# Kernel tuning notes

Hardware: AMD Instinct MI355X
Metric: run time of the kernel (lower is better)

Reference implementation:

```python
import jax, jax.numpy as jnp
import numpy as np

R = 2          # pool ratio -> context window = R * P
P = 8          # patch_size
STRIDE = 8     # window_stride
NH = 8         # n_heads
EPS = 1e-6


def _partition_nonoverlap(x, ws):
    # (N,C,H,W) -> (N*nH*nW, C, ws, ws), matches F.unfold path with padding 0
    n, c, h, w = x.shape
    x = x.reshape(n, c, h // ws, ws, w // ws, ws)
    x = jnp.transpose(x, (0, 2, 4, 1, 3, 5))
    return x.reshape(-1, c, ws, ws)


def _partition_overlap(x, ws, stride):
    # (N,C,H,W) -> (N*nH*nW, C, ws, ws) with padding (ws-stride)//2, matching F.unfold
    n, c, h, w = x.shape
    pad = (ws - stride) // 2
    xp = jnp.pad(x, ((0, 0), (0, 0), (pad, pad), (pad, pad)))
    ih = (jnp.arange(h // stride) * stride)[:, None] + jnp.arange(ws)[None, :]
    iw = (jnp.arange(w // stride) * stride)[:, None] + jnp.arange(ws)[None, :]
    xw = xp[:, :, ih, :]          # (n, c, nH, ws, Wp)
    xw = xw[:, :, :, :, iw]       # (n, c, nH, ws, nW, ws)
    xw = jnp.transpose(xw, (0, 2, 4, 1, 3, 5))  # (n, nH, nW, c, ws, ws)
    return xw.reshape(-1, c, ws, ws)


def setup_inputs() -> dict:
    key = jax.random.key(0)
    ks = jax.random.split(key, 4)
    C = 512
    x = jax.random.normal(ks[0], (1, C, 128, 128), jnp.float32)
    ln_w = jnp.ones((C,), jnp.float32)
    ln_b = jnp.zeros((C,), jnp.float32)
    mix_w = jax.random.normal(ks[1], (NH, P * P, P * P), jnp.float32) * 0.02
    mix_b = jnp.zeros((NH, P * P), jnp.float32)
    in_w = jax.random.normal(ks[2], (3 * C, C), jnp.float32) * 0.02
    in_b = jnp.zeros((3 * C,), jnp.float32)
    out_w = jax.random.normal(ks[3], (C, C), jnp.float32) * 0.02
    out_b = jnp.zeros((C,), jnp.float32)
    return dict(x=x, ln_w=ln_w, ln_b=ln_b, mix_w=mix_w, mix_b=mix_b,
                in_w=in_w, in_b=in_b, out_w=out_w, out_b=out_b)


def reference(x, ln_w, ln_b, mix_w, mix_b, in_w, in_b, out_w, out_b):
    n, c, h, w = x.shape
    ws = R * P
    L = P * P  # 64 positions per window

    # query windows: non-overlapping 8x8 patches -> (B, L, C)
    q = _partition_nonoverlap(x, P)
    q = q.reshape(-1, c, L).transpose(0, 2, 1)

    # context windows: 16x16 overlapping, avg-pooled r x r -> 8x8 -> (B, L, C)
    ctx = _partition_overlap(x, ws, STRIDE)
    ctx = ctx.reshape(-1, c, P, R, P, R).mean(axis=(3, 5))  # AvgPool2d(r, r)
    ctx = ctx.reshape(-1, c, L).transpose(0, 2, 1)

    # LayerNorm over channel dim (eps 1e-6, biased variance)
    mu = ctx.mean(-1, keepdims=True)
    var = ctx.var(-1, keepdims=True)
    ctx = (ctx - mu) / jnp.sqrt(var + EPS) * ln_w + ln_b

    # PositionMixing: per-head Linear(64,64) over the L axis + residual
    B = ctx.shape[0]
    t = ctx.transpose(0, 2, 1).reshape(B, NH, c // NH, L)  # (B, H, hd, L)
    mixed = jnp.einsum('bhcl,hml->bhcm', t, mix_w) + mix_b[None, :, None, :]
    ctx = (t + mixed).reshape(B, c, L).transpose(0, 2, 1)  # (B, L, C)

    # nn.MultiheadAttention with batch_first=False (torch default):
    # first dim B (windows) is the SEQUENCE, second dim L=64 is the BATCH.
    hd = c // NH
    Wq, Wk, Wv = in_w[:c], in_w[c:2 * c], in_w[2 * c:]
    bq, bk, bv = in_b[:c], in_b[c:2 * c], in_b[2 * c:]
    Q = (jnp.einsum('slc,ec->sle', q, Wq) + bq).reshape(B, L, NH, hd)
    K = (jnp.einsum('slc,ec->sle', ctx, Wk) + bk).reshape(B, L, NH, hd)
    V = (jnp.einsum('slc,ec->sle', ctx, Wv) + bv).reshape(B, L, NH, hd)
    scale = 1.0 / jnp.sqrt(jnp.asarray(hd, x.dtype))
    scores = jnp.einsum('slhd,tlhd->lhst', Q, K) * scale  # (L, H, B, B)
    attn = jax.nn.softmax(scores, axis=-1)
    o = jnp.einsum('lhst,tlhd->slhd', attn, V).reshape(B, L, c)
    o = jnp.einsum('slc,ec->sle', o, out_w) + out_b

    # nlc_to_nchw + window_reverse -> (N, C, H, W)
    o = o.transpose(0, 2, 1).reshape(B, c, P, P)
    o = o.reshape(n, h // P, w // P, c, P, P)
    o = jnp.transpose(o, (0, 3, 1, 4, 2, 5)).reshape(n, c, h, w)
    return o
```

## Files before the change

kernel.cpp:

```cpp
#include <hip/hip_runtime.h>


typedef __bf16 bf16;
typedef __bf16 bf16x2 __attribute__((ext_vector_type(2)));
typedef __bf16 bf16x4 __attribute__((ext_vector_type(4)));
typedef __bf16 bf16x8 __attribute__((ext_vector_type(8)));
typedef float f32x4 __attribute__((ext_vector_type(4)));

#define MFMA(a, b, c) __builtin_amdgcn_mfma_f32_16x16x32_bf16(a, b, c, 0, 0, 0)

__device__ __forceinline__ void gll16(const void* g, void* l) {
  __builtin_amdgcn_global_load_lds((const __attribute__((address_space(1))) void*)g,
                                   (__attribute__((address_space(3))) void*)l, 16, 0, 0);
}

__global__ void k_wconv(const float* __restrict__ in_w, const float* __restrict__ out_w,
                        bf16* __restrict__ wib, bf16* __restrict__ wob) {
  int i = blockIdx.x * blockDim.x + threadIdx.x;
  const int n1 = (1536 * 512) / 4;
  float4 v;
  bf16* dst;
  if (i < n1) { v = ((const float4*)in_w)[i];      dst = wib + (size_t)i * 4; }
  else        { v = ((const float4*)out_w)[i - n1]; dst = wob + (size_t)(i - n1) * 4; }
  dst[0] = (bf16)v.x; dst[1] = (bf16)v.y; dst[2] = (bf16)v.z; dst[3] = (bf16)v.w;
}

__global__ __launch_bounds__(256) void k_pq(const float* __restrict__ x,
                                            float* __restrict__ xp2t,
                                            bf16* __restrict__ qb) {
  __shared__ float xs[2][64][133];
  const int y2 = blockIdx.x, c0 = blockIdx.y * 64, t = threadIdx.x;
  #pragma unroll
  for (int it = 0; it < 16; ++it) {
    int flat = it * 256 + t;
    int ci = flat >> 6, rest = flat & 63;
    int yb = rest >> 5, xq = rest & 31;
    float4 v = *(const float4*)(x + (size_t)(c0 + ci) * 16384 +
                                (size_t)(2 * y2 + yb) * 128 + xq * 4);
    float* d = &xs[yb][ci][xq * 4];
    d[0] = v.x; d[1] = v.y; d[2] = v.z; d[3] = v.w;
  }
  __syncthreads();
  #pragma unroll
  for (int it = 0; it < 16; ++it) {
    int flat = it * 256 + t;
    int x2 = flat >> 6, ci = flat & 63;
    float s = xs[0][ci][2 * x2] + xs[0][ci][2 * x2 + 1] +
              xs[1][ci][2 * x2] + xs[1][ci][2 * x2 + 1];
    xp2t[(size_t)(y2 * 64 + x2) * 512 + c0 + ci] = 0.25f * s;
  }
  #pragma unroll
  for (int yb = 0; yb < 2; ++yb) {
    const int Y = 2 * y2 + yb;
    const int hy = Y >> 3, py = Y & 7;
    #pragma unroll
    for (int it = 0; it < 32; ++it) {
      int flat = it * 256 + t;
      int X = flat >> 6, ci = flat & 63;
      int l = py * 8 + (X & 7), s = hy * 16 + (X >> 3);
      qb[((size_t)l * 256 + s) * 512 + c0 + ci] = (bf16)xs[yb][ci][X];
    }
  }
}

__global__ __launch_bounds__(512) void k_ln(const float* __restrict__ xp2t,
                                            const float* __restrict__ lnw,
                                            const float* __restrict__ lnb,
                                            bf16* __restrict__ T) {
  __shared__ bf16 Tt[512][24];
  const int s = blockIdx.x, qt = blockIdx.y;
  const int wy = s >> 4, wx = s & 15;
  const int t = threadIdx.x, wv = t >> 6, ln = t & 63;

  float wl[8], bl[8];
  #pragma unroll
  for (int k = 0; k < 8; ++k) { wl[k] = lnw[k * 64 + ln]; bl[k] = lnb[k * 64 + ln]; }

  float v[2][8], mu_[2], rs_[2];
  #pragma unroll
  for (int p = 0; p < 2; ++p) {
    const int l = qt * 16 + wv * 2 + p;
    const int py = l >> 3, px = l & 7;
    const int y2 = wy * 4 - 2 + py, x2 = wx * 4 - 2 + px;
    const bool inb = (y2 >= 0) && (y2 < 64) && (x2 >= 0) && (x2 < 64);
    const float* src = xp2t + (size_t)(y2 * 64 + x2) * 512;
    float sum = 0.f, ssq = 0.f;
    #pragma unroll
    for (int k = 0; k < 8; ++k) {
      float xv = 0.f;
      if (inb) xv = src[k * 64 + ln];
      v[p][k] = xv; sum += xv; ssq += xv * xv;
    }
    #pragma unroll
    for (int off = 1; off < 64; off <<= 1) {
      sum += __shfl_xor(sum, off);
      ssq += __shfl_xor(ssq, off);
    }
    float mu = sum * (1.f / 512.f);
    mu_[p] = mu;
    rs_[p] = rsqrtf(ssq * (1.f / 512.f) - mu * mu + 1e-6f);
  }
  #pragma unroll
  for (int k = 0; k < 8; ++k) {
    const int c = k * 64 + ln;
    bf16x2 u;
    u.x = (bf16)((v[0][k] - mu_[0]) * rs_[0] * wl[k] + bl[k]);
    u.y = (bf16)((v[1][k] - mu_[1]) * rs_[1] * wl[k] + bl[k]);
    *(bf16x2*)(&Tt[c][wv * 2]) = u;
  }
  __syncthreads();
  #pragma unroll
  for (int it = 0; it < 2; ++it) {
    int flat = it * 512 + t;
    int c = flat >> 1, ch = flat & 1;
    bf16x8 u = *(const bf16x8*)(&Tt[c][ch * 8]);
    *(bf16x8*)(T + ((size_t)s * 512 + c) * 64 + qt * 16 + ch * 8) = u;
  }
}

__global__ __launch_bounds__(256) void k_mix(const bf16* __restrict__ T,
                                             const float* __restrict__ mix_w,
                                             const float* __restrict__ mix_b,
                                             bf16* __restrict__ ctx) {
  const int t = threadIdx.x, wv = t >> 6, ln = t & 63;
  const int s = blockIdx.x, hg = blockIdx.y;
  const int h = hg * 4 + wv;
  const int q = ln >> 4, r = ln & 15;

  bf16x8 a[4][2];
  #pragma unroll
  for (int m = 0; m < 4; ++m) {
    #pragma unroll
    for (int ks = 0; ks < 2; ++ks) {
      const int rm = m * 16 + r;
      const float* wsrc = mix_w + ((size_t)h * 64 + rm) * 64 + ks * 32 + q * 8;
      bf16x8 pk;
      #pragma unroll
      for (int e = 0; e < 8; ++e) {
        int l = ks * 32 + q * 8 + e;
        float w = wsrc[e] + (rm == l ? 1.f : 0.f);
        pk[e] = (bf16)w;
      }
      a[m][ks] = pk;
    }
  }
  const bf16* Tb = T + ((size_t)s * 512 + h * 64) * 64;
  bf16x8 b[4][2];
  #pragma unroll
  for (int n = 0; n < 4; ++n) {
    #pragma unroll
    for (int ks = 0; ks < 2; ++ks)
      b[n][ks] = *(const bf16x8*)(Tb + (size_t)(n * 16 + r) * 64 + ks * 32 + q * 8);
  }
  f32x4 acc[4][4] = {};
  #pragma unroll
  for (int ks = 0; ks < 2; ++ks) {
    #pragma unroll
    for (int m = 0; m < 4; ++m) {
      #pragma unroll
      for (int n = 0; n < 4; ++n) acc[m][n] = MFMA(a[m][ks], b[n][ks], acc[m][n]);
    }
  }
  #pragma unroll
  for (int m = 0; m < 4; ++m) {
    #pragma unroll
    for (int j = 0; j < 4; ++j) {
      const int rm = m * 16 + q * 4 + j;
      const float bias = mix_b[h * 64 + rm];
      #pragma unroll
      for (int n = 0; n < 4; ++n)
        ctx[((size_t)rm * 256 + s) * 512 + h * 64 + n * 16 + r] =
            (bf16)(acc[m][n][j] + bias);
    }
  }
}

template <int MODE>
__global__ __launch_bounds__(256, 3) void k_gemm(const bf16* __restrict__ A,
                                                 const bf16* __restrict__ B,
                                                 const float* __restrict__ bias,
                                                 bf16* __restrict__ O0,
                                                 bf16* __restrict__ O1) {
  __shared__ bf16 As[4096];
  __shared__ bf16 Bs[4096];
  const int t = threadIdx.x, wv = t >> 6, ln = t & 63;
  const int bm = blockIdx.y, bn = blockIdx.x;
  const int wm = wv >> 1, wn = wv & 1;
  f32x4 acc[4][4] = {};

  const int srow = wv * 32 + (ln >> 2);
  const int scolb = (ln & 3) * 16;
  const char* ga = (const char*)A + ((size_t)(bm * 128 + srow) * 512) * 2 + scolb;
  const char* gb = (const char*)B + ((size_t)(bn * 128 + srow) * 512) * 2 + scolb;
  bf16* lA = As + wv * 1024;
  bf16* lB = Bs + wv * 1024;

  for (int k0 = 0; k0 < 512; k0 += 32) {
    gll16(ga + k0 * 2,             lA);
    gll16(ga + k0 * 2 + 16 * 1024, lA + 512);
    gll16(gb + k0 * 2,             lB);
    gll16(gb + k0 * 2 + 16 * 1024, lB + 512);
    __syncthreads();
    bf16x8 af[4], bfr[4];
    #pragma unroll
    for (int m = 0; m < 4; ++m)
      af[m] = *(const bf16x8*)(As + (wm * 64 + m * 16 + (ln & 15)) * 32 + (ln >> 4) * 8);
    #pragma unroll
    for (int n = 0; n < 4; ++n)
      bfr[n] = *(const bf16x8*)(Bs + (wn * 64 + n * 16 + (ln & 15)) * 32 + (ln >> 4) * 8);
    #pragma unroll
    for (int m = 0; m < 4; ++m) {
      #pragma unroll
      for (int n = 0; n < 4; ++n) acc[m][n] = MFMA(af[m], bfr[n], acc[m][n]);
    }
    __syncthreads();
  }

  const int r0 = bm * 128 + wm * 64 + (ln >> 4) * 4;
  const int c0 = bn * 128 + wn * 64 + (ln & 15);
  #pragma unroll
  for (int m = 0; m < 4; ++m) {
    const int rg0 = r0 + m * 16;
    #pragma unroll
    for (int n = 0; n < 4; ++n) {
      const int cg = c0 + n * 16;
      const float bv = bias[cg];
      if constexpr (MODE == 2) {
        #pragma unroll
        for (int j = 0; j < 4; ++j)
          O0[(size_t)(rg0 + j) * 512 + cg] = (bf16)(acc[m][n][j] + bv);
      } else if constexpr (MODE == 0) {
        const int li = rg0 >> 8;
        #pragma unroll
        for (int j = 0; j < 4; ++j) {
          int sp = (rg0 + j) & 255;
          O0[(((size_t)li * 8 + (cg >> 6)) * 256 + sp) * 64 + (cg & 63)] =
              (bf16)(acc[m][n][j] + bv);
        }
      } else {
        const int li = rg0 >> 8;
        if (cg < 512) {
          #pragma unroll
          for (int j = 0; j < 4; ++j) {
            int sp = (rg0 + j) & 255;
            O0[(((size_t)li * 8 + (cg >> 6)) * 256 + sp) * 64 + (cg & 63)] =
                (bf16)(acc[m][n][j] + bv);
          }
        } else {
          const int e = cg - 512, hh = e >> 6, d = e & 63;
          const int sp = rg0 & 255;
          bf16x4 pk;
          #pragma unroll
          for (int j = 0; j < 4; ++j) pk[j] = (bf16)(acc[m][n][j] + bv);
          *(bf16x4*)(&O1[(((size_t)li * 8 + hh) * 64 + d) * 256 + sp]) = pk;
        }
      }
    }
  }
}

__global__ __launch_bounds__(256, 4) void k_attn(const bf16* __restrict__ Qa,
                                                 const bf16* __restrict__ Ka,
                                                 const bf16* __restrict__ Vt,
                                                 bf16* __restrict__ Oa) {
  __shared__ bf16 Ks[128][68];
  __shared__ bf16 Ps[64][132];
  __shared__ float sfl[64];
  __shared__ float rrs[64];

  const int t = threadIdx.x, wv = t >> 6, ln = t & 63;
  const int q = ln >> 4, r = ln & 15;
  const int bid = blockIdx.x;
  const int st = (bid >> 3) & 3;
  const int lh = (bid & 7) | ((bid >> 5) << 3);
  const int s0 = st * 64;
  const size_t base = (size_t)lh * (256 * 64);
  const bf16* Qlh = Qa + base;
  const bf16* Klh = Ka + base;
  const bf16* Vlh = Vt + base;

  const float SC = 0.125f * 1.4426950408889634f;

  bf16x8 aq[2];
  #pragma unroll
  for (int ks = 0; ks < 2; ++ks)
    aq[ks] = *(const bf16x8*)(Qlh + (size_t)(s0 + wv * 16 + r) * 64 + ks * 32 + q * 8);

  const int krow = t >> 1, khf = (t & 1) * 32;
  {
    bf16x8 kst0[4];
    #pragma unroll
    for (int i = 0; i < 4; ++i)
      kst0[i] = *(const bf16x8*)(Klh + (size_t)krow * 64 + khf + i * 8);
    #pragma unroll
    for (int i = 0; i < 4; ++i) *(bf16x8*)(&Ks[krow][khf + i * 8]) = kst0[i];
  }
  __syncthreads();

  f32x4 ao[4] = {};
  float m4[4], l4[4];
  f32x4 acc[8];

  #pragma unroll
  for (int n = 0; n < 8; ++n) acc[n] = (f32x4){0.f, 0.f, 0.f, 0.f};
  #pragma unroll
  for (int n = 0; n < 8; ++n) {
    bf16x8 b0 = *(const bf16x8*)(&Ks[n * 16 + r][q * 8]);
    bf16x8 b1 = *(const bf16x8*)(&Ks[n * 16 + r][32 + q * 8]);
    acc[n] = MFMA(aq[0], b0, acc[n]);
    acc[n] = MFMA(aq[1], b1, acc[n]);
  }

  bf16x8 bv[4];
  #pragma unroll
  for (int ks = 0; ks < 4; ++ks)
    bv[ks] = *(const bf16x8*)(Vlh + (size_t)(wv * 16 + r) * 256 + ks * 32 + q * 8);
  bf16x8 kst[4];
  #pragma unroll
  for (int i = 0; i < 4; ++i)
    kst[i] = *(const bf16x8*)(Klh + (size_t)(128 + krow) * 64 + khf + i * 8);

  #pragma unroll
  for (int j = 0; j < 4; ++j) {
    float mx = acc[0][j];
    #pragma unroll
    for (int n = 1; n < 8; ++n) mx = fmaxf(mx, acc[n][j]);
    #pragma unroll
    for (int off = 1; off < 16; off <<= 1) mx = fmaxf(mx, __shfl_xor(mx, off));
    m4[j] = mx;
    const float ms = mx * SC;
    float sm = 0.f;
    #pragma unroll
    for (int n = 0; n < 8; ++n) {
      float p = exp2f(acc[n][j] * SC - ms);
      acc[n][j] = p;
      sm += p;
    }
    #pragma unroll
    for (int off = 1; off < 16; off <<= 1) sm += __shfl_xor(sm, off);
    l4[j] = sm;
    const int row = wv * 16 + q * 4 + j;
    #pragma unroll
    for (int n = 0; n < 8; ++n) Ps[row][n * 16 + r] = (bf16)acc[n][j];
  }
  __syncthreads();

  #pragma unroll
  for (int i = 0; i < 4; ++i) *(bf16x8*)(&Ks[krow][khf + i * 8]) = kst[i];
  #pragma unroll
  for (int ks = 0; ks < 4; ++ks) {
    #pragma unroll
    for (int m = 0; m < 4; ++m) {
      bf16x8 ap = *(const bf16x8*)(&Ps[m * 16 + r][ks * 32 + q * 8]);
      ao[m] = MFMA(ap, bv[ks], ao[m]);
    }
  }
  __syncthreads();

  #pragma unroll
  for (int n = 0; n < 8; ++n) acc[n] = (f32x4){0.f, 0.f, 0.f, 0.f};
  #pragma unroll
  for (int n = 0; n < 8; ++n) {
    bf16x8 b0 = *(const bf16x8*)(&Ks[n * 16 + r][q * 8]);
    bf16x8 b1 = *(const bf16x8*)(&Ks[n * 16 + r][32 + q * 8]);
    acc[n] = MFMA(aq[0], b0, acc[n]);
    acc[n] = MFMA(aq[1], b1, acc[n]);
  }
  #pragma unroll
  for (int ks = 0; ks < 4; ++ks)
    bv[ks] = *(const bf16x8*)(Vlh + (size_t)(wv * 16 + r) * 256 + 128 + ks * 32 + q * 8);

  float sf4[4], rr4[4];
  #pragma unroll
  for (int j = 0; j < 4; ++j) {
    float mx = acc[0][j];
    #pragma unroll
    for (int n = 1; n < 8; ++n) mx = fmaxf(mx, acc[n][j]);
    #pragma unroll
    for (int off = 1; off < 16; off <<= 1) mx = fmaxf(mx, __shfl_xor(mx, off));
    const float mn = fmaxf(m4[j], mx);
    const float sf = exp2f((m4[j] - mn) * SC);
    const float ms = mn * SC;
    float sm = 0.f;
    #pragma unroll
    for (int n = 0; n < 8; ++n) {
      float p = exp2f(acc[n][j] * SC - ms);
      acc[n][j] = p;
      sm += p;
    }
    #pragma unroll
    for (int off = 1; off < 16; off <<= 1) sm += __shfl_xor(sm, off);
    sf4[j] = sf;
    rr4[j] = 1.f / (l4[j] * sf + sm);
    const int row = wv * 16 + q * 4 + j;
    #pragma unroll
    for (int n = 0; n < 8; ++n) Ps[row][n * 16 + r] = (bf16)acc[n][j];
  }
  if (r == 0) {
    *(f32x4*)(&sfl[wv * 16 + q * 4]) = (f32x4){sf4[0], sf4[1], sf4[2], sf4[3]};
    *(f32x4*)(&rrs[wv * 16 + q * 4]) = (f32x4){rr4[0], rr4[1], rr4[2], rr4[3]};
  }
  __syncthreads();

  #pragma unroll
  for (int m = 0; m < 4; ++m) {
    f32x4 sv = *(const f32x4*)(&sfl[m * 16 + q * 4]);
    #pragma unroll
    for (int j = 0; j < 4; ++j) ao[m][j] *= sv[j];
  }
  #pragma unroll
  for (int ks = 0; ks < 4; ++ks) {
    #pragma unroll
    for (int m = 0; m < 4; ++m) {
      bf16x8 ap = *(const bf16x8*)(&Ps[m * 16 + r][ks * 32 + q * 8]);
      ao[m] = MFMA(ap, bv[ks], ao[m]);
    }
  }

  float(*FS)[68] = (float(*)[68])(&Ks[0][0]);
  #pragma unroll
  for (int m = 0; m < 4; ++m) {
    f32x4 rv = *(const f32x4*)(&rrs[m * 16 + q * 4]);
    #pragma unroll
    for (int j = 0; j < 4; ++j)
      FS[m * 16 + q * 4 + j][wv * 16 + r] = ao[m][j] * rv[j];
  }
  __syncthreads();

  {
    const int row = t >> 2, qq = t & 3;
    const float* srcp = &FS[row][qq * 16];
    bf16x8 o0, o1;
    #pragma unroll
    for (int i = 0; i < 8; ++i) o0[i] = (bf16)srcp[i];
    #pragma unroll
    for (int i = 0; i < 8; ++i) o1[i] = (bf16)srcp[8 + i];
    bf16* dst = Oa + ((size_t)(lh >> 3) * 256 + s0 + row) * 512 + (lh & 7) * 64 + qq * 16;
    *(bf16x8*)(dst) = o0;
    *(bf16x8*)(dst + 8) = o1;
  }
}

__global__ void k_orelay(const bf16* __restrict__ o_tmp, float* __restrict__ out) {
  __shared__ bf16 buf[64][130];
  const int hy = blockIdx.x, py = blockIdx.y, e0 = blockIdx.z * 64, t = threadIdx.x;
  #pragma unroll
  for (int i = 0; i < 32; ++i) {
    int flat = i * 256 + t;
    int r = flat >> 6, e = flat & 63;
    int px = r >> 4, hx = r & 15;
    buf[e][hx * 8 + px] =
        o_tmp[((size_t)(py * 8 + px) * 256 + hy * 16 + hx) * 512 + e0 + e];
  }
  __syncthreads();
  const int Y = hy * 8 + py;
  #pragma unroll
  for (int i = 0; i < 32; ++i) {
    int flat = i * 256 + t;
    int e = flat >> 7, X = flat & 127;
    out[(size_t)(e0 + e) * 16384 + (size_t)Y * 128 + X] = (float)buf[e][X];
  }
}

extern "C" void kernel_launch(void* const* d_in, const int* in_sizes, int n_in,
                              void* d_out, int out_size, void* d_ws, size_t ws_size,
                              hipStream_t stream) {
  const float* x     = (const float*)d_in[0];
  const float* ln_w  = (const float*)d_in[1];
  const float* ln_b  = (const float*)d_in[2];
  const float* mix_w = (const float*)d_in[3];
  const float* mix_b = (const float*)d_in[4];
  const float* in_w  = (const float*)d_in[5];
  const float* in_b  = (const float*)d_in[6];
  const float* out_w = (const float*)d_in[7];
  const float* out_b = (const float*)d_in[8];
  float* out = (float*)d_out;
  char* ws = (char*)d_ws;

  const size_t MB = 1u << 20;
  float* xp2t = (float*)(ws);
  bf16* qb    = (bf16*)(ws + 8 * MB);
  bf16* Tn    = (bf16*)(ws + 24 * MB);
  bf16* ctxb  = (bf16*)(ws + 40 * MB);
  bf16* Qa    = (bf16*)(ws + 56 * MB);
  bf16* Ka    = (bf16*)(ws);
  bf16* Vt    = (bf16*)(ws + 16 * MB);
  bf16* oatt  = (bf16*)(ws + 32 * MB);
  bf16* otmp  = (bf16*)(ws + 48 * MB);
  bf16* wib   = (bf16*)(ws + 72 * MB);
  bf16* wob   = (bf16*)(ws + 72 * MB + 1572864);

  k_wconv<<<1024, 256, 0, stream>>>(in_w, out_w, wib, wob);
  k_pq<<<dim3(64, 8), 256, 0, stream>>>(x, xp2t, qb);
  k_ln<<<dim3(256, 4), 512, 0, stream>>>(xp2t, ln_w, ln_b, Tn);
  k_mix<<<dim3(256, 2), 256, 0, stream>>>(Tn, mix_w, mix_b, ctxb);
  k_gemm<0><<<dim3(4, 128), 256, 0, stream>>>(qb, wib, in_b, Qa, nullptr);
  k_gemm<1><<<dim3(8, 128), 256, 0, stream>>>(ctxb, wib + 512 * 512, in_b + 512, Ka, Vt);
  k_attn<<<2048, 256, 0, stream>>>(Qa, Ka, Vt, oatt);
  k_gemm<2><<<dim3(4, 128), 256, 0, stream>>>(oatt, wob, out_b, otmp, nullptr);
  k_orelay<<<dim3(16, 8, 8), 256, 0, stream>>>(otmp, out);
}
```

Before: 153.4 us.

## Deepen GEMM K-tile to 64 with XOR-swizzled LDS and swap grid axes

The GEMM kernel now stages a 128x64 K-slice per iteration instead of 128x32, halving the number of barrier pairs. Rows in shared memory are XOR-swizzled in 16-byte chunks so the fragment reads avoid bank conflicts. The grid is transposed so consecutive blocks walk M with a fixed weight tile, which should improve L2 reuse of the weights. LDS use doubles to 32 KB per block while the launch bound now asks for 4 blocks per CU, which may cost occupancy or registers.

```diff
diff --git a/kernel.cpp b/kernel.cpp
--- a/kernel.cpp
+++ b/kernel.cpp
@@ -176,48 +176,53 @@
 }
 
 template <int MODE>
-__global__ __launch_bounds__(256, 3) void k_gemm(const bf16* __restrict__ A,
+__global__ __launch_bounds__(256, 4) void k_gemm(const bf16* __restrict__ A,
                                                  const bf16* __restrict__ B,
                                                  const float* __restrict__ bias,
                                                  bf16* __restrict__ O0,
                                                  bf16* __restrict__ O1) {
-  __shared__ bf16 As[4096];
-  __shared__ bf16 Bs[4096];
+  __shared__ bf16 As[8192];
+  __shared__ bf16 Bs[8192];
   const int t = threadIdx.x, wv = t >> 6, ln = t & 63;
-  const int bm = blockIdx.y, bn = blockIdx.x;
+  const int bm = blockIdx.x, bn = blockIdx.y;
   const int wm = wv >> 1, wn = wv & 1;
+  const int q = ln >> 4, r = ln & 15;
   f32x4 acc[4][4] = {};
 
-  const int srow = wv * 32 + (ln >> 2);
-  const int scolb = (ln & 3) * 16;
-  const char* ga = (const char*)A + ((size_t)(bm * 128 + srow) * 512) * 2 + scolb;
-  const char* gb = (const char*)B + ((size_t)(bn * 128 + srow) * 512) * 2 + scolb;
-  bf16* lA = As + wv * 1024;
-  bf16* lB = Bs + wv * 1024;
-
-  for (int k0 = 0; k0 < 512; k0 += 32) {
-    gll16(ga + k0 * 2,             lA);
-    gll16(ga + k0 * 2 + 16 * 1024, lA + 512);
-    gll16(gb + k0 * 2,             lB);
-    gll16(gb + k0 * 2 + 16 * 1024, lB + 512);
+  const int srow = wv * 8 + (ln >> 3);
+  const int swzc = (ln & 7) ^ (ln >> 3);
+  const char* ga = (const char*)A + ((size_t)(bm * 128 + srow) * 512) * 2 + swzc * 16;
+  const char* gb = (const char*)B + ((size_t)(bn * 128 + srow) * 512) * 2 + swzc * 16;
+
+  for (int k0 = 0; k0 < 512; k0 += 64) {
+    #pragma unroll
+    for (int i = 0; i < 4; ++i) {
+      gll16(ga + (size_t)i * 32 * 1024 + k0 * 2, As + i * 2048 + wv * 512);
+      gll16(gb + (size_t)i * 32 * 1024 + k0 * 2, Bs + i * 2048 + wv * 512);
+    }
     __syncthreads();
-    bf16x8 af[4], bfr[4];
-    #pragma unroll
-    for (int m = 0; m < 4; ++m)
-      af[m] = *(const bf16x8*)(As + (wm * 64 + m * 16 + (ln & 15)) * 32 + (ln >> 4) * 8);
-    #pragma unroll
-    for (int n = 0; n < 4; ++n)
-      bfr[n] = *(const bf16x8*)(Bs + (wn * 64 + n * 16 + (ln & 15)) * 32 + (ln >> 4) * 8);
-    #pragma unroll
-    for (int m = 0; m < 4; ++m) {
+    #pragma unroll
+    for (int ks = 0; ks < 2; ++ks) {
+      bf16x8 af[4], bfr[4];
       #pragma unroll
-      for (int n = 0; n < 4; ++n) acc[m][n] = MFMA(af[m], bfr[n], acc[m][n]);
+      for (int m = 0; m < 4; ++m)
+        af[m] = *(const bf16x8*)(As + (wm * 64 + m * 16 + r) * 64 +
+                                 (((ks * 4 + q) ^ (r & 7)) * 8));
+      #pragma unroll
+      for (int n = 0; n < 4; ++n)
+        bfr[n] = *(const bf16x8*)(Bs + (wn * 64 + n * 16 + r) * 64 +
+                                  (((ks * 4 + q) ^ (r & 7)) * 8));
+      #pragma unroll
+      for (int m = 0; m < 4; ++m) {
+        #pragma unroll
+        for (int n = 0; n < 4; ++n) acc[m][n] = MFMA(af[m], bfr[n], acc[m][n]);
+      }
     }
     __syncthreads();
   }
 
-  const int r0 = bm * 128 + wm * 64 + (ln >> 4) * 4;
-  const int c0 = bn * 128 + wn * 64 + (ln & 15);
+  const int r0 = bm * 128 + wm * 64 + q * 4;
+  const int c0 = bn * 128 + wn * 64 + r;
   #pragma unroll
   for (int m = 0; m < 4; ++m) {
     const int rg0 = r0 + m * 16;
@@ -494,9 +499,9 @@
   k_pq<<<dim3(64, 8), 256, 0, stream>>>(x, xp2t, qb);
   k_ln<<<dim3(256, 4), 512, 0, stream>>>(xp2t, ln_w, ln_b, Tn);
   k_mix<<<dim3(256, 2), 256, 0, stream>>>(Tn, mix_w, mix_b, ctxb);
-  k_gemm<0><<<dim3(4, 128), 256, 0, stream>>>(qb, wib, in_b, Qa, nullptr);
-  k_gemm<1><<<dim3(8, 128), 256, 0, stream>>>(ctxb, wib + 512 * 512, in_b + 512, Ka, Vt);
+  k_gemm<0><<<dim3(128, 4), 256, 0, stream>>>(qb, wib, in_b, Qa, nullptr);
+  k_gemm<1><<<dim3(128, 8), 256, 0, stream>>>(ctxb, wib + 512 * 512, in_b + 512, Ka, Vt);
   k_attn<<<2048, 256, 0, stream>>>(Qa, Ka, Vt, oatt);
-  k_gemm<2><<<dim3(4, 128), 256, 0, stream>>>(oatt, wob, out_b, otmp, nullptr);
+  k_gemm<2><<<dim3(128, 4), 256, 0, stream>>>(oatt, wob, out_b, otmp, nullptr);
   k_orelay<<<dim3(16, 8, 8), 256, 0, stream>>>(otmp, out);
 }
```

New measurement: 138.6 us. -9.7%, faster.
